# Kernel optimization log

Hardware: AMD Instinct MI355X
Metric: run time of the kernel (lower is better)

Reference implementation:

```python
import jax, jax.numpy as jnp
import numpy as np

NEG_SLOPE = 0.2  # PyG GATConv default leaky_relu slope


def _gat_layer(x, src, dst, n_nodes, W, a_src, a_dst, b, heads, out_ch):
    # x: [N, Fin] -> h: [N, H, C]
    h = (x @ W).reshape(n_nodes, heads, out_ch)
    alpha_s = jnp.einsum('nhc,hc->nh', h, a_src)  # [N, H]
    alpha_d = jnp.einsum('nhc,hc->nh', h, a_dst)  # [N, H]
    e = jax.nn.leaky_relu(alpha_s[src] + alpha_d[dst], NEG_SLOPE)  # [E, H]
    # segment softmax over edges grouped by destination node
    m = jax.ops.segment_max(e, dst, num_segments=n_nodes)          # [N, H]
    e = jnp.exp(e - m[dst])
    denom = jax.ops.segment_sum(e, dst, num_segments=n_nodes)      # [N, H]
    alpha = e / denom[dst]                                          # self-loops guarantee denom > 0
    msg = alpha[:, :, None] * h[src]                                # [E, H, C]
    out = jax.ops.segment_sum(msg, dst, num_segments=n_nodes)      # [N, H, C]
    return out.reshape(n_nodes, heads * out_ch) + b


def reference(x, edge_index, batch, W1, a_src1, a_dst1, b1, W2, a_src2, a_dst2, b2, fc_w, fc_b):
    n_nodes = x.shape[0]
    heads = a_src1.shape[0]
    # PyG GATConv adds self-loops by default
    loops = jnp.arange(n_nodes, dtype=edge_index.dtype)
    src = jnp.concatenate([edge_index[0], loops])
    dst = jnp.concatenate([edge_index[1], loops])

    h = _gat_layer(x, src, dst, n_nodes, W1, a_src1, a_dst1, b1, heads, 64)
    h = jax.nn.relu(h)  # dropout is identity in eval mode
    h = _gat_layer(h, src, dst, n_nodes, W2, a_src2, a_dst2, b2, heads, 16)
    h = jax.nn.relu(h)

    n_graphs = 64
    sums = jax.ops.segment_sum(h, batch, num_segments=n_graphs)                    # [G, 64]
    counts = jax.ops.segment_sum(jnp.ones((n_nodes,), h.dtype), batch, num_segments=n_graphs)
    pooled = sums / jnp.maximum(counts, 1.0)[:, None]                              # global_mean_pool
    return pooled @ fc_w + fc_b


def setup_inputs() -> dict:
    key = jax.random.key(0)
    ks = jax.random.split(key, 12)
    N, E, F_in, G = 50000, 800000, 128, 64
    H = 4
    x = jax.random.normal(ks[0], (N, F_in), jnp.float32)
    edge_index = jax.random.randint(ks[1], (2, E), 0, N, jnp.int32)
    batch = jnp.sort(jax.random.randint(ks[2], (N,), 0, G, jnp.int32))
    s1 = 1.0 / np.sqrt(F_in)
    s2 = 1.0 / np.sqrt(H * 64)
    s3 = 1.0 / np.sqrt(H * 16)
    return {
        'x': x,
        'edge_index': edge_index,
        'batch': batch,
        'W1': jax.random.normal(ks[3], (F_in, H * 64), jnp.float32) * s1,
        'a_src1': jax.random.normal(ks[4], (H, 64), jnp.float32) * s1,
        'a_dst1': jax.random.normal(ks[5], (H, 64), jnp.float32) * s1,
        'b1': jnp.zeros((H * 64,), jnp.float32),
        'W2': jax.random.normal(ks[6], (H * 64, H * 16), jnp.float32) * s2,
        'a_src2': jax.random.normal(ks[7], (H, 16), jnp.float32) * s2,
        'a_dst2': jax.random.normal(ks[8], (H, 16), jnp.float32) * s2,
        'b2': jnp.zeros((H * 16,), jnp.float32),
        'fc_w': jax.random.normal(ks[9], (H * 16, 32), jnp.float32) * s3,
        'fc_b': jnp.zeros((32,), jnp.float32),
    }
```

## Files before the change

### kernel.cpp

```cpp
#include <hip/hip_runtime.h>
#include <hip/hip_bf16.h>
#include <hip/hip_fp16.h>
#include <math.h>

#define HEADS 4
#define CAP 64

typedef _Float16 half8_t __attribute__((ext_vector_type(8)));
typedef float float4_t __attribute__((ext_vector_type(4)));


__global__ __launch_bounds__(256) void prep_k(int* cnt, unsigned short* slots, int N, int NB,
                                              const float* __restrict__ W1, _Float16* __restrict__ W1T,
                                              const float* __restrict__ W2, _Float16* __restrict__ W2T) {
    int bx = blockIdx.x;
    if (bx < NB) {
        int i = bx * 256 + threadIdx.x;
        if (i < N) {
            cnt[i] = 1;
            slots[(size_t)i * CAP] = (unsigned short)i;
        }
    } else if (bx < NB + 128) {
        int k = bx - NB;
        int n = threadIdx.x;
        W1T[n * 128 + k] = (_Float16)W1[k * 256 + n];
    } else {
        int n = bx - NB - 128;
        int k = threadIdx.x;
        W2T[n * 256 + k] = (_Float16)W2[k * 64 + n];
    }
}


__global__ __launch_bounds__(256) void fused_scatter_gemm1_k(
    const int* __restrict__ src, const int* __restrict__ dst,
    int* __restrict__ cnt, unsigned short* __restrict__ slots, int E, int SB,
    const float* __restrict__ A,
    const _Float16* __restrict__ BT,
    __half* __restrict__ hout,
    const float* __restrict__ avs,
    const float* __restrict__ avd,
    float* __restrict__ os,
    float* __restrict__ od, int M) {
    __shared__ _Float16 lds[4 * 16 * 72];

    if ((int)blockIdx.x < SB) {
        int T = SB * 256;
        int t0 = blockIdx.x * 256 + threadIdx.x;
        int d[8], s[8];
        #pragma unroll
        for (int k = 0; k < 8; k++) {
            int i = t0 + k * T;
            if (i < E) { d[k] = dst[i]; s[k] = src[i]; }
            else d[k] = -1;
        }
        int p[8];
        #pragma unroll
        for (int k = 0; k < 8; k++) {
            if (d[k] >= 0) p[k] = atomicAdd(&cnt[d[k]], 1);
        }
        #pragma unroll
        for (int k = 0; k < 8; k++) {
            if (d[k] >= 0 && p[k] < CAP)
                slots[(size_t)d[k] * CAP + p[k]] = (unsigned short)s[k];
        }
        return;
    }

    int bx = blockIdx.x - SB;
    int wave = threadIdx.x >> 6;
    int lane = threadIdx.x & 63;
    int q = lane >> 4;
    int c16 = lane & 15;
    int row0 = bx * 64 + wave * 16;

    half8_t a[4];
    int ar = row0 + c16;
    bool avalid = (ar < M);
    const float* ap = A + (size_t)ar * 128;
    #pragma unroll
    for (int ks = 0; ks < 4; ks++) {
        if (avalid) {
            float4 f0 = *(const float4*)(ap + ks * 32 + q * 8);
            float4 f1 = *(const float4*)(ap + ks * 32 + q * 8 + 4);
            half8_t h;
            h[0] = (_Float16)f0.x; h[1] = (_Float16)f0.y;
            h[2] = (_Float16)f0.z; h[3] = (_Float16)f0.w;
            h[4] = (_Float16)f1.x; h[5] = (_Float16)f1.y;
            h[6] = (_Float16)f1.z; h[7] = (_Float16)f1.w;
            a[ks] = h;
        } else {
            a[ks] = (half8_t)(_Float16)0.0f;
        }
    }

    float4_t acc[16];
    #pragma unroll
    for (int ct = 0; ct < 16; ct++) acc[ct] = (float4_t)0.f;

    #pragma unroll
    for (int ks = 0; ks < 4; ks++) {
        #pragma unroll
        for (int ct = 0; ct < 16; ct++) {
            half8_t b = *(const half8_t*)(BT + (size_t)(ct * 16 + c16) * 128 + ks * 32 + q * 8);
            acc[ct] = __builtin_amdgcn_mfma_f32_16x16x32_f16(a[ks], b, acc[ct], 0, 0, 0);
        }
    }

    float psh[4][4] = {}, pdh[4][4] = {};
    #pragma unroll
    for (int ct = 0; ct < 16; ct++) {
        int h = ct >> 2;
        int cih = (ct & 3) * 16 + c16;
        float as_v = avs[h * 64 + cih];
        float ad_v = avd[h * 64 + cih];
        #pragma unroll
        for (int r = 0; r < 4; r++) {
            psh[h][r] = fmaf(acc[ct][r], as_v, psh[h][r]);
            pdh[h][r] = fmaf(acc[ct][r], ad_v, pdh[h][r]);
        }
    }
    #pragma unroll
    for (int h = 0; h < 4; h++) {
        #pragma unroll
        for (int r = 0; r < 4; r++) {
            #pragma unroll
            for (int o = 8; o >= 1; o >>= 1) {
                psh[h][r] += __shfl_down(psh[h][r], o, 16);
                pdh[h][r] += __shfl_down(pdh[h][r], o, 16);
            }
        }
    }
    if (c16 == 0) {
        #pragma unroll
        for (int r = 0; r < 4; r++) {
            int gr = row0 + q * 4 + r;
            if (gr < M) {
                #pragma unroll
                for (int h = 0; h < 4; h++) {
                    os[(size_t)gr * HEADS + h] = psh[h][r];
                    od[(size_t)gr * HEADS + h] = pdh[h][r];
                }
            }
        }
    }

    _Float16* wl = lds + wave * (16 * 72);
    #pragma unroll
    for (int chunk = 0; chunk < 4; chunk++) {
        #pragma unroll
        for (int c4 = 0; c4 < 4; c4++) {
            int ct = chunk * 4 + c4;
            #pragma unroll
            for (int r = 0; r < 4; r++) {
                wl[(q * 4 + r) * 72 + c4 * 16 + c16] = (_Float16)acc[ct][r];
            }
        }
        __syncthreads();
        #pragma unroll
        for (int pass = 0; pass < 2; pass++) {
            int idx8 = pass * 64 + lane;
            int row = idx8 >> 3;
            int col8 = idx8 & 7;
            int gr = row0 + row;
            if (gr < M) {
                *(half8_t*)(hout + (size_t)gr * 256 + chunk * 64 + col8 * 8) =
                    *(const half8_t*)(wl + row * 72 + col8 * 8);
            }
        }
        __syncthreads();
    }
}


__global__ __launch_bounds__(256) void mfma_gemm2_k(
    const _Float16* __restrict__ Ah,
    const _Float16* __restrict__ BT,
    __half* __restrict__ hout,
    const float* __restrict__ avs,
    const float* __restrict__ avd,
    float* __restrict__ os,
    float* __restrict__ od, int M) {
    __shared__ _Float16 lds[4 * 16 * 64];
    int wave = threadIdx.x >> 6;
    int lane = threadIdx.x & 63;
    int q = lane >> 4;
    int c16 = lane & 15;
    int row0 = blockIdx.x * 64 + wave * 16;

    half8_t a[8];
    int ar = row0 + c16;
    bool avalid = (ar < M);
    const _Float16* ap = Ah + (size_t)ar * 256;
    #pragma unroll
    for (int ks = 0; ks < 8; ks++) {
        if (avalid) a[ks] = *(const half8_t*)(ap + ks * 32 + q * 8);
        else        a[ks] = (half8_t)(_Float16)0.0f;
    }

    float4_t acc[4];
    #pragma unroll
    for (int ct = 0; ct < 4; ct++) acc[ct] = (float4_t)0.f;

    #pragma unroll
    for (int ks = 0; ks < 8; ks++) {
        #pragma unroll
        for (int ct = 0; ct < 4; ct++) {
            half8_t b = *(const half8_t*)(BT + (size_t)(ct * 16 + c16) * 256 + ks * 32 + q * 8);
            acc[ct] = __builtin_amdgcn_mfma_f32_16x16x32_f16(a[ks], b, acc[ct], 0, 0, 0);
        }
    }

    float ps[4][4], pd[4][4];
    #pragma unroll
    for (int ct = 0; ct < 4; ct++) {
        float as_v = avs[ct * 16 + c16];
        float ad_v = avd[ct * 16 + c16];
        #pragma unroll
        for (int r = 0; r < 4; r++) {
            ps[ct][r] = acc[ct][r] * as_v;
            pd[ct][r] = acc[ct][r] * ad_v;
            #pragma unroll
            for (int o = 8; o >= 1; o >>= 1) {
                ps[ct][r] += __shfl_down(ps[ct][r], o, 16);
                pd[ct][r] += __shfl_down(pd[ct][r], o, 16);
            }
        }
    }
    if (c16 == 0) {
        #pragma unroll
        for (int r = 0; r < 4; r++) {
            int gr = row0 + q * 4 + r;
            if (gr < M) {
                #pragma unroll
                for (int ct = 0; ct < 4; ct++) {
                    os[(size_t)gr * HEADS + ct] = ps[ct][r];
                    od[(size_t)gr * HEADS + ct] = pd[ct][r];
                }
            }
        }
    }

    _Float16* wl = lds + wave * (16 * 64);
    #pragma unroll
    for (int ct = 0; ct < 4; ct++) {
        #pragma unroll
        for (int r = 0; r < 4; r++) {
            wl[(q * 4 + r) * 64 + ct * 16 + c16] = (_Float16)acc[ct][r];
        }
    }
    __syncthreads();
    #pragma unroll
    for (int pass = 0; pass < 2; pass++) {
        int idx8 = pass * 64 + lane;
        int row = idx8 >> 3;
        int col8 = idx8 & 7;
        int gr = row0 + row;
        if (gr < M) {
            *(half8_t*)(hout + (size_t)gr * 64 + col8 * 8) =
                *(const half8_t*)(wl + row * 64 + col8 * 8);
        }
    }
}


__global__ __launch_bounds__(256) void gat_agg64_f16_k(
    const __half* __restrict__ hsrc,
    const float* __restrict__ as,
    const float* __restrict__ ad,
    const int* __restrict__ cnt,
    const unsigned short* __restrict__ slots,
    const float* __restrict__ bias,
    __half* __restrict__ outh,
    int N) {
    int node = blockIdx.x * 4 + (threadIdx.x >> 6);
    if (node >= N) return;
    int l = threadIdx.x & 63;
    int h = l >> 4;
    int je = l & 15;
    int hb = h << 4;
    int deg = min(cnt[node], CAP);
    const unsigned short* sp = slots + (size_t)node * CAP;
    float adh = ad[(size_t)node * HEADS + h];
    float4 bv = *(const float4*)(bias + l * 4);
    float m = -INFINITY, den = 0.f;
    float4 acc = make_float4(0.f, 0.f, 0.f, 0.f);
    for (int base = 0; base < deg; base += 16) {
        int cl = min(16, deg - base);
        int s = 0;
        float e = -INFINITY;
        if (je < cl) {
            s = sp[base + je];
            float a = as[(size_t)s * HEADS + h] + adh;
            e = (a > 0.f) ? a : 0.2f * a;
        }
        float cmax = e;
        #pragma unroll
        for (int o = 8; o >= 1; o >>= 1) cmax = fmaxf(cmax, __shfl_xor(cmax, o));
        float m_new = fmaxf(m, cmax);
        float p = (je < cl) ? __expf(e - m_new) : 0.f;
        float sum = p;
        #pragma unroll
        for (int o = 8; o >= 1; o >>= 1) sum += __shfl_xor(sum, o);
        float sc = __expf(m - m_new);
        den = den * sc + sum;
        m = m_new;
        acc.x *= sc; acc.y *= sc; acc.z *= sc; acc.w *= sc;
        int j = 0;
        for (; j + 4 <= cl; j += 4) {
            float p0 = __shfl(p, hb + j),     p1 = __shfl(p, hb + j + 1);
            float p2 = __shfl(p, hb + j + 2), p3 = __shfl(p, hb + j + 3);
            int s0 = __shfl(s, hb + j),     s1 = __shfl(s, hb + j + 1);
            int s2 = __shfl(s, hb + j + 2), s3 = __shfl(s, hb + j + 3);
            uint2 r0 = *(const uint2*)(hsrc + (size_t)s0 * 256 + l * 4);
            uint2 r1 = *(const uint2*)(hsrc + (size_t)s1 * 256 + l * 4);
            uint2 r2 = *(const uint2*)(hsrc + (size_t)s2 * 256 + l * 4);
            uint2 r3 = *(const uint2*)(hsrc + (size_t)s3 * 256 + l * 4);
            float2 a0 = __half22float2(*(__half2*)&r0.x), b0 = __half22float2(*(__half2*)&r0.y);
            float2 a1 = __half22float2(*(__half2*)&r1.x), b1 = __half22float2(*(__half2*)&r1.y);
            float2 a2 = __half22float2(*(__half2*)&r2.x), b2 = __half22float2(*(__half2*)&r2.y);
            float2 a3 = __half22float2(*(__half2*)&r3.x), b3 = __half22float2(*(__half2*)&r3.y);
            acc.x = fmaf(p0, a0.x, acc.x); acc.y = fmaf(p0, a0.y, acc.y);
            acc.z = fmaf(p0, b0.x, acc.z); acc.w = fmaf(p0, b0.y, acc.w);
            acc.x = fmaf(p1, a1.x, acc.x); acc.y = fmaf(p1, a1.y, acc.y);
            acc.z = fmaf(p1, b1.x, acc.z); acc.w = fmaf(p1, b1.y, acc.w);
            acc.x = fmaf(p2, a2.x, acc.x); acc.y = fmaf(p2, a2.y, acc.y);
            acc.z = fmaf(p2, b2.x, acc.z); acc.w = fmaf(p2, b2.y, acc.w);
            acc.x = fmaf(p3, a3.x, acc.x); acc.y = fmaf(p3, a3.y, acc.y);
            acc.z = fmaf(p3, b3.x, acc.z); acc.w = fmaf(p3, b3.y, acc.w);
        }
        for (; j < cl; j++) {
            float pj = __shfl(p, hb + j);
            int sj = __shfl(s, hb + j);
            uint2 r0 = *(const uint2*)(hsrc + (size_t)sj * 256 + l * 4);
            float2 a0 = __half22float2(*(__half2*)&r0.x), b0 = __half22float2(*(__half2*)&r0.y);
            acc.x = fmaf(pj, a0.x, acc.x); acc.y = fmaf(pj, a0.y, acc.y);
            acc.z = fmaf(pj, b0.x, acc.z); acc.w = fmaf(pj, b0.y, acc.w);
        }
    }
    float inv = 1.f / den;
    float rx = fmaxf(fmaf(acc.x, inv, bv.x), 0.f);
    float ry = fmaxf(fmaf(acc.y, inv, bv.y), 0.f);
    float rz = fmaxf(fmaf(acc.z, inv, bv.z), 0.f);
    float rw = fmaxf(fmaf(acc.w, inv, bv.w), 0.f);
    __half2* op = (__half2*)(outh + (size_t)node * 256 + l * 4);
    op[0] = __floats2half2_rn(rx, ry);
    op[1] = __floats2half2_rn(rz, rw);
}


__global__ __launch_bounds__(256) void gat_agg16_f16_k(
    const __half* __restrict__ hsrc,
    const float* __restrict__ as,
    const float* __restrict__ ad,
    const int* __restrict__ cnt,
    const unsigned short* __restrict__ slots,
    const float* __restrict__ bias,
    float* __restrict__ out, int N) {
    int node = blockIdx.x * 4 + (threadIdx.x >> 6);
    if (node >= N) return;
    int l = threadIdx.x & 63;
    int ha = l >> 4;
    int je = l & 15;
    int q = l & 15;
    int hh = q >> 2;
    int eg = l >> 4;
    int deg = min(cnt[node], CAP);
    const unsigned short* sp = slots + (size_t)node * CAP;
    float adh = ad[(size_t)node * HEADS + ha];
    float m = -INFINITY, den = 0.f;
    float4 acc = make_float4(0.f, 0.f, 0.f, 0.f);
    for (int base = 0; base < deg; base += 16) {
        int cl = min(16, deg - base);
        int s = 0;
        float e = -INFINITY;
        if (je < cl) {
            s = sp[base + je];
            float a = as[(size_t)s * HEADS + ha] + adh;
            e = (a > 0.f) ? a : 0.2f * a;
        }
        float cmax = e;
        #pragma unroll
        for (int o = 8; o >= 1; o >>= 1) cmax = fmaxf(cmax, __shfl_xor(cmax, o));
        float m_new = fmaxf(m, cmax);
        float p = (je < cl) ? __expf(e - m_new) : 0.f;
        float sum = p;
        #pragma unroll
        for (int o = 8; o >= 1; o >>= 1) sum += __shfl_xor(sum, o);
        float sc = __expf(m - m_new);
        den = den * sc + sum;
        m = m_new;
        float sch = __shfl(sc, hh << 4);
        acc.x *= sch; acc.y *= sch; acc.z *= sch; acc.w *= sch;

        int jbase = eg * 4;
        float pj[4]; int sj[4]; bool vj[4];
        #pragma unroll
        for (int jj = 0; jj < 4; jj++) {
            int j = jbase + jj;
            int jc = min(j, cl - 1);
            pj[jj] = __shfl(p, (hh << 4) + jc);
            sj[jj] = __shfl(s, (hh << 4) + jc);
            vj[jj] = (j < cl);
        }
        uint2 rv[4];
        #pragma unroll
        for (int jj = 0; jj < 4; jj++) {
            if (vj[jj]) rv[jj] = *(const uint2*)(hsrc + (size_t)sj[jj] * 64 + q * 4);
        }
        #pragma unroll
        for (int jj = 0; jj < 4; jj++) {
            if (vj[jj]) {
                float2 f0 = __half22float2(*(__half2*)&rv[jj].x);
                float2 f1 = __half22float2(*(__half2*)&rv[jj].y);
                acc.x = fmaf(pj[jj], f0.x, acc.x); acc.y = fmaf(pj[jj], f0.y, acc.y);
                acc.z = fmaf(pj[jj], f1.x, acc.z); acc.w = fmaf(pj[jj], f1.y, acc.w);
            }
        }
    }
    acc.x += __shfl_xor(acc.x, 16); acc.y += __shfl_xor(acc.y, 16);
    acc.z += __shfl_xor(acc.z, 16); acc.w += __shfl_xor(acc.w, 16);
    acc.x += __shfl_xor(acc.x, 32); acc.y += __shfl_xor(acc.y, 32);
    acc.z += __shfl_xor(acc.z, 32); acc.w += __shfl_xor(acc.w, 32);
    float denh = __shfl(den, hh << 4);
    if (eg == 0) {
        float inv = 1.f / denh;
        float4 bv = *(const float4*)(bias + q * 4);
        float4 r;
        r.x = fmaxf(fmaf(acc.x, inv, bv.x), 0.f);
        r.y = fmaxf(fmaf(acc.y, inv, bv.y), 0.f);
        r.z = fmaxf(fmaf(acc.z, inv, bv.z), 0.f);
        r.w = fmaxf(fmaf(acc.w, inv, bv.w), 0.f);
        *(float4*)(out + (size_t)node * 64 + q * 4) = r;
    }
}


__global__ __launch_bounds__(256) void bounds_zero_k(const int* __restrict__ batch, int N,
                                                     int* __restrict__ bstart,
                                                     float* __restrict__ sums) {
    int t = threadIdx.x;
    if (t <= 64) {
        int lo = 0, hi = N;
        while (lo < hi) {
            int mid = (lo + hi) >> 1;
            if (batch[mid] < t) lo = mid + 1; else hi = mid;
        }
        bstart[t] = lo;
    }
    for (int i = t; i < 64 * 64; i += 256) sums[i] = 0.f;
}

__global__ __launch_bounds__(256) void pool_sum_k(const float* __restrict__ g2,
                                                  const int* __restrict__ batch,
                                                  float* __restrict__ sums, int N) {
    int c = threadIdx.x & 63;
    int r = threadIdx.x >> 6;
    int base = blockIdx.x * 256;
    int lim = min(base + 256, N);
    float acc = 0.f;
    int cur = -1;
    for (int n = base + r; n < lim; n += 4) {
        int g = batch[n];
        if (g != cur) {
            if (cur >= 0) atomicAdd(&sums[cur * 64 + c], acc);
            acc = 0.f;
            cur = g;
        }
        acc += g2[(size_t)n * 64 + c];
    }
    if (cur >= 0) atomicAdd(&sums[cur * 64 + c], acc);
}

__global__ void fc_k(const float* __restrict__ sums, const int* __restrict__ bstart,
                     const float* __restrict__ w, const float* __restrict__ b,
                     float* __restrict__ out) {
    int g = blockIdx.x, o = threadIdx.x;
    float cnt_ = (float)max(bstart[g + 1] - bstart[g], 1);
    float inv = 1.f / cnt_;
    float acc = b[o];
    for (int k = 0; k < 64; k++) acc = fmaf(sums[g * 64 + k] * inv, w[k * 32 + o], acc);
    out[g * 32 + o] = acc;
}


static inline size_t align_up(size_t x, size_t a) { return (x + a - 1) & ~(a - 1); }

extern "C" void kernel_launch(void* const* d_in, const int* in_sizes, int n_in,
                              void* d_out, int out_size, void* d_ws, size_t ws_size,
                              hipStream_t stream) {
    const float* x      = (const float*)d_in[0];
    const int*   ei     = (const int*)d_in[1];
    const int*   batch  = (const int*)d_in[2];
    const float* W1     = (const float*)d_in[3];
    const float* a_src1 = (const float*)d_in[4];
    const float* a_dst1 = (const float*)d_in[5];
    const float* b1     = (const float*)d_in[6];
    const float* W2     = (const float*)d_in[7];
    const float* a_src2 = (const float*)d_in[8];
    const float* a_dst2 = (const float*)d_in[9];
    const float* b2     = (const float*)d_in[10];
    const float* fc_w   = (const float*)d_in[11];
    const float* fc_b   = (const float*)d_in[12];
    float* out = (float*)d_out;

    const int N = in_sizes[2];
    const int E = in_sizes[1] / 2;
    const int F_in = in_sizes[0] / N;
    const int D1 = HEADS * 64;
    const int D2 = HEADS * 16;

    const int* src = ei;
    const int* dst = ei + E;

    char* w = (char*)d_ws;
    size_t off = 0;
    auto alloc = [&](size_t bytes) {
        size_t p = off;
        off = align_up(off + bytes, 256);
        return (void*)(w + p);
    };
    int* cnt    = (int*)alloc((size_t)N * 4);
    unsigned short* slots = (unsigned short*)alloc((size_t)N * CAP * 2);
    int* bstart = (int*)alloc(65 * 4);
    float* pooled = (float*)alloc(64 * 64 * 4);
    float* as1  = (float*)alloc((size_t)N * HEADS * 4);
    float* ad1  = (float*)alloc((size_t)N * HEADS * 4);
    float* as2  = (float*)alloc((size_t)N * HEADS * 4);
    float* ad2  = (float*)alloc((size_t)N * HEADS * 4);
    __half* h1h = (__half*)alloc((size_t)N * D1 * 2);
    __half* g1h = (__half*)alloc((size_t)N * D1 * 2);
    __half* h2h = (__half*)alloc((size_t)N * D2 * 2);
    float* g2   = (float*)alloc((size_t)N * D2 * 4);
    _Float16* w1t = (_Float16*)alloc((size_t)F_in * D1 * 2);
    _Float16* w2t = (_Float16*)alloc((size_t)D1 * D2 * 2);

    const int NB = (N + 255) / 256;
    prep_k<<<NB + 128 + 64, 256, 0, stream>>>(cnt, slots, N, NB, W1, w1t, W2, w2t);

    const int SB = (E + 2047) / 2048;
    const int GB = (N + 63) / 64;
    fused_scatter_gemm1_k<<<SB + GB, 256, 0, stream>>>(
        src, dst, cnt, slots, E, SB,
        x, w1t, h1h, a_src1, a_dst1, as1, ad1, N);

    gat_agg64_f16_k<<<(N + 3) / 4, 256, 0, stream>>>(h1h, as1, ad1, cnt, slots, b1, g1h, N);

    mfma_gemm2_k<<<(N + 63) / 64, 256, 0, stream>>>((const _Float16*)g1h, w2t, h2h,
                                                    a_src2, a_dst2, as2, ad2, N);
    gat_agg16_f16_k<<<(N + 3) / 4, 256, 0, stream>>>(h2h, as2, ad2, cnt, slots, b2, g2, N);

    bounds_zero_k<<<1, 256, 0, stream>>>(batch, N, bstart, pooled);
    pool_sum_k<<<(N + 255) / 256, 256, 0, stream>>>(g2, batch, pooled, N);
    fc_k<<<64, 32, 0, stream>>>(pooled, bstart, fc_w, fc_b, out);
}
```

Before: 314.8 us.

## Replace global-atomic edge bucketing with chunked LDS counting, scan, and placement

Edge bucketing by destination no longer uses global atomics on per-node counters. It now runs in three passes: 128 chunk blocks build per-chunk 8-bit destination histograms in shared memory, a column scan turns them into per-chunk offsets and total counts, and a placement pass writes slots using shared-memory atomic ranks. This removes contended global atomics, but it adds two kernel launches, a 6.4MB byte-count buffer, and only 128 blocks for the counting and placement work. The scatter also no longer overlaps with GEMM1 in the same launch, and placement becomes deterministic in edge order.

Result: slower. 346.2 us (+10.0%).

```diff
diff --git a/kernel.cpp b/kernel.cpp
--- a/kernel.cpp
+++ b/kernel.cpp
@@ -5,36 +5,111 @@
 
 #define HEADS 4
 #define CAP 64
+#define NC 128
 
 typedef _Float16 half8_t __attribute__((ext_vector_type(8)));
 typedef float float4_t __attribute__((ext_vector_type(4)));
 
 
-__global__ __launch_bounds__(256) void prep_k(int* cnt, unsigned short* slots, int N, int NB,
+__global__ __launch_bounds__(256) void prep_k(unsigned short* slots, int N, int NB,
                                               const float* __restrict__ W1, _Float16* __restrict__ W1T,
-                                              const float* __restrict__ W2, _Float16* __restrict__ W2T) {
+                                              const float* __restrict__ W2, _Float16* __restrict__ W2T,
+                                              const int* __restrict__ dst, int E,
+                                              unsigned char* __restrict__ cnts8, int NS) {
+    __shared__ unsigned int sh[12544];
     int bx = blockIdx.x;
     if (bx < NB) {
         int i = bx * 256 + threadIdx.x;
-        if (i < N) {
-            cnt[i] = 1;
-            slots[(size_t)i * CAP] = (unsigned short)i;
-        }
+        if (i < N) slots[(size_t)i * CAP] = (unsigned short)i;
     } else if (bx < NB + 128) {
         int k = bx - NB;
         int n = threadIdx.x;
         W1T[n * 128 + k] = (_Float16)W1[k * 256 + n];
-    } else {
+    } else if (bx < NB + 192) {
         int n = bx - NB - 128;
         int k = threadIdx.x;
         W2T[n * 256 + k] = (_Float16)W2[k * 64 + n];
-    }
-}
-
-
-__global__ __launch_bounds__(256) void fused_scatter_gemm1_k(
-    const int* __restrict__ src, const int* __restrict__ dst,
-    int* __restrict__ cnt, unsigned short* __restrict__ slots, int E, int SB,
+    } else {
+        int c = bx - NB - 192;
+        int nw = (N + 3) >> 2;
+        for (int i = threadIdx.x; i < nw; i += 256) sh[i] = 0u;
+        __syncthreads();
+        int epc = (E + NC - 1) / NC;
+        int lo = c * epc, hi = min(lo + epc, E);
+        for (int i = lo + threadIdx.x; i < hi; i += 256) {
+            int d = dst[i];
+            atomicAdd(&sh[d >> 2], 1u << ((d & 3) * 8));
+        }
+        __syncthreads();
+        unsigned int* row32 = (unsigned int*)(cnts8 + (size_t)c * NS);
+        for (int i = threadIdx.x; i < nw; i += 256) row32[i] = sh[i];
+    }
+}
+
+
+__global__ __launch_bounds__(256) void scan_chunks_k(unsigned char* __restrict__ cnts8,
+                                                     int NS, int N, int* __restrict__ cnt) {
+    int d4 = (blockIdx.x * 256 + threadIdx.x) * 4;
+    if (d4 >= N) return;
+    if (d4 + 3 < N) {
+        unsigned int a0 = 1, a1 = 1, a2 = 1, a3 = 1;
+        unsigned char* base = cnts8 + d4;
+        unsigned int v = *(unsigned int*)base;
+        for (int c = 0; c < NC; c++) {
+            unsigned int vn = 0;
+            if (c + 1 < NC) vn = *(unsigned int*)(base + (size_t)(c + 1) * NS);
+            unsigned int o = min(a0, 255u) | (min(a1, 255u) << 8) |
+                             (min(a2, 255u) << 16) | (min(a3, 255u) << 24);
+            *(unsigned int*)(base + (size_t)c * NS) = o;
+            a0 += v & 255u; a1 += (v >> 8) & 255u;
+            a2 += (v >> 16) & 255u; a3 += (v >> 24) & 255u;
+            v = vn;
+        }
+        cnt[d4]     = (int)a0;
+        cnt[d4 + 1] = (int)a1;
+        cnt[d4 + 2] = (int)a2;
+        cnt[d4 + 3] = (int)a3;
+    } else {
+        for (int k = 0; k < 4; k++) {
+            int d = d4 + k;
+            if (d >= N) break;
+            unsigned int a = 1;
+            for (int c = 0; c < NC; c++) {
+                unsigned char* p = cnts8 + (size_t)c * NS + d;
+                unsigned int vv = *p;
+                *p = (unsigned char)min(a, 255u);
+                a += vv;
+            }
+            cnt[d] = (int)a;
+        }
+    }
+}
+
+
+__global__ __launch_bounds__(256) void place_k(const int* __restrict__ src,
+                                               const int* __restrict__ dst, int E,
+                                               const unsigned char* __restrict__ offs8, int NS,
+                                               unsigned short* __restrict__ slots, int N) {
+    __shared__ unsigned int sh[12544];
+    int c = blockIdx.x;
+    int nw = (N + 3) >> 2;
+    for (int i = threadIdx.x; i < nw; i += 256) sh[i] = 0u;
+    __syncthreads();
+    int epc = (E + NC - 1) / NC;
+    int lo = c * epc, hi = min(lo + epc, E);
+    const unsigned char* offr = offs8 + (size_t)c * NS;
+    for (int i = lo + threadIdx.x; i < hi; i += 256) {
+        int d = dst[i];
+        int s = src[i];
+        unsigned int sh_old = atomicAdd(&sh[d >> 2], 1u << ((d & 3) * 8));
+        int rank = (int)((sh_old >> ((d & 3) * 8)) & 255u);
+        int pos = (int)offr[d] + rank;
+        if (pos < CAP) slots[(size_t)d * CAP + pos] = (unsigned short)s;
+    }
+}
+
+
+__global__ __launch_bounds__(256) void mfma_gemm1_k(
     const float* __restrict__ A,
     const _Float16* __restrict__ BT,
     __half* __restrict__ hout,
@@ -44,30 +119,7 @@
     float* __restrict__ od, int M) {
     __shared__ _Float16 lds[4 * 16 * 72];
 
-    if ((int)blockIdx.x < SB) {
-        int T = SB * 256;
-        int t0 = blockIdx.x * 256 + threadIdx.x;
-        int d[8], s[8];
-        #pragma unroll
-        for (int k = 0; k < 8; k++) {
-            int i = t0 + k * T;
-            if (i < E) { d[k] = dst[i]; s[k] = src[i]; }
-            else d[k] = -1;
-        }
-        int p[8];
-        #pragma unroll
-        for (int k = 0; k < 8; k++) {
-            if (d[k] >= 0) p[k] = atomicAdd(&cnt[d[k]], 1);
-        }
-        #pragma unroll
-        for (int k = 0; k < 8; k++) {
-            if (d[k] >= 0 && p[k] < CAP)
-                slots[(size_t)d[k] * CAP + p[k]] = (unsigned short)s[k];
-        }
-        return;
-    }
-
-    int bx = blockIdx.x - SB;
+    int bx = blockIdx.x;
     int wave = threadIdx.x >> 6;
     int lane = threadIdx.x & 63;
     int q = lane >> 4;
@@ -509,6 +561,7 @@
     const int F_in = in_sizes[0] / N;
     const int D1 = HEADS * 64;
     const int D2 = HEADS * 16;
+    const int NS = (N + 3) & ~3;
 
     const int* src = ei;
     const int* dst = ei + E;
@@ -534,15 +587,18 @@
     float* g2   = (float*)alloc((size_t)N * D2 * 4);
     _Float16* w1t = (_Float16*)alloc((size_t)F_in * D1 * 2);
     _Float16* w2t = (_Float16*)alloc((size_t)D1 * D2 * 2);
+    unsigned char* cnts8 = (unsigned char*)alloc((size_t)NC * NS);
 
     const int NB = (N + 255) / 256;
-    prep_k<<<NB + 128 + 64, 256, 0, stream>>>(cnt, slots, N, NB, W1, w1t, W2, w2t);
-
-    const int SB = (E + 2047) / 2048;
+    prep_k<<<NB + 192 + NC, 256, 0, stream>>>(slots, N, NB, W1, w1t, W2, w2t,
+                                              dst, E, cnts8, NS);
+
+    scan_chunks_k<<<(N + 1023) / 1024, 256, 0, stream>>>(cnts8, NS, N, cnt);
+
+    place_k<<<NC, 256, 0, stream>>>(src, dst, E, cnts8, NS, slots, N);
+
     const int GB = (N + 63) / 64;
-    fused_scatter_gemm1_k<<<SB + GB, 256, 0, stream>>>(
-        src, dst, cnt, slots, E, SB,
-        x, w1t, h1h, a_src1, a_dst1, as1, ad1, N);
+    mfma_gemm1_k<<<GB, 256, 0, stream>>>(x, w1t, h1h, a_src1, a_dst1, as1, ad1, N);
 
     gat_agg64_f16_k<<<(N + 3) / 4, 256, 0, stream>>>(h1h, as1, ad1, cnt, slots, b1, g1h, N);
 
```
